# Kernel optimization log

Hardware: AMD Instinct MI355X
Metric: run time of the kernel (lower is better)

The kernel has to match this reference:

```python
import jax, jax.numpy as jnp
import numpy as np

INF = 1.0e7   # matches torch INF = 1.0 * 10000000.0
EOS_ID = 2
FIN_INIT = -1.0e9  # finite stand-in for torch's -inf init of fin_log_probs


def setup_inputs() -> dict:
    key = jax.random.key(0)
    k1, k2, k3, k4, k5, k6 = jax.random.split(key, 6)
    P, D, S, V = 32, 8, 2048, 128000
    # next-token probability distribution per (prompt, draft)
    logits = jax.random.normal(k1, (P * D, V), dtype=jnp.float32)
    probs = jax.nn.softmax(logits, axis=-1)
    alive_seq = jax.random.randint(k2, (P, D, S), 0, V, dtype=jnp.int32)
    fin_seq = jax.random.randint(k3, (P, D, S), 0, V, dtype=jnp.int32)
    alive_log_probs = -5.0 * jax.random.uniform(k4, (P, D), dtype=jnp.float32)
    fin_log_probs = jnp.full((P, D), FIN_INIT, dtype=jnp.float32)
    still_prompt = jax.random.randint(k5, (P,), 0, 2) == 1
    is_first = jax.random.randint(k6, (P,), 0, 2) == 1
    return {"probs": probs, "alive_seq": alive_seq, "fin_seq": fin_seq,
            "alive_log_probs": alive_log_probs, "fin_log_probs": fin_log_probs,
            "still_prompt": still_prompt, "is_first": is_first, "cur_pos": 1024}


def reference(probs, alive_seq, fin_seq, alive_log_probs, fin_log_probs,
              still_prompt, is_first, cur_pos):
    P, D = alive_log_probs.shape
    V = probs.shape[-1]
    # log-prob accumulation (smoothing=None path)
    log_probs = jnp.log(probs.reshape(P, D, V))                  # (P, D, V)
    curr = alive_log_probs[:, :, None] + log_probs               # (P, D, V)
    # joint topk over beams*vocab
    flat = curr.reshape(P, D * V)
    topk_lp, topk_i = jax.lax.top_k(flat, 2 * D)                 # (P, 2D)
    topk_beam_id = topk_i // V
    topk_tok = topk_i % V
    # first-generation override: only beam 0 counts
    f_vals, f_idx = jax.lax.top_k(log_probs[:, 0, :], 2 * D)     # (P, 2D)
    m = is_first[:, None]
    topk_tok = jnp.where(m, f_idx, topk_tok)
    topk_lp = jnp.where(m, alive_log_probs[:, 0:1] + f_vals, topk_lp)
    # gather parent sequences, write new token at cur_pos
    topk_seq = jnp.take_along_axis(alive_seq, topk_beam_id[:, :, None], axis=1)
    topk_seq = topk_seq.at[:, :, cur_pos].set(topk_tok)
    topk_finished = topk_tok == EOS_ID
    # grow_alive: keep best unfinished
    alive_masked = topk_lp + topk_finished * (-INF)
    na_lp, na_idx = jax.lax.top_k(alive_masked, D)               # (P, D)
    na_seq = jnp.take_along_axis(topk_seq, na_idx[:, :, None], axis=1)
    attention_change_ids = jnp.take_along_axis(topk_beam_id, na_idx, axis=1)
    # grow_fin: keep best finished among old + new
    fin_masked = topk_lp + (~topk_finished) * (-INF)
    cat_seq = jnp.concatenate([fin_seq, topk_seq], axis=1)       # (P, 3D, S)
    cat_lp = jnp.concatenate([fin_log_probs, fin_masked], axis=1)
    nf_lp, nf_idx = jax.lax.top_k(cat_lp, D)
    nf_seq = jnp.take_along_axis(cat_seq, nf_idx[:, :, None], axis=1)
    # still-prompt masking: keep old state, identity attention ids
    sp = still_prompt
    attention_change_ids = jnp.where(sp[:, None], jnp.arange(D), attention_change_ids)
    new_alive_seq = jnp.where(sp[:, None, None], alive_seq, na_seq)
    new_alive_lp = jnp.where(sp[:, None], alive_log_probs, na_lp)
    new_fin_seq = jnp.where(sp[:, None, None], fin_seq, nf_seq)
    new_fin_lp = jnp.where(sp[:, None], fin_log_probs, nf_lp)
    return (attention_change_ids, new_alive_seq, new_alive_lp, new_fin_seq, new_fin_lp)
```

## Files before the change

### kernel.cpp

```cpp
#include <hip/hip_runtime.h>
#include <stdint.h>

#define NEG_BIG -3.0e38f
#define INF_ 10000000.0f
#define EOS_ID 2
#define V_DIM 128000
#define S_DIM 2048
#define CAP 2048

__device__ __forceinline__ bool better(float v1, int i1, float v2, int i2) {
    return (v1 > v2) || (v1 == v2 && i1 < i2);
}
__device__ __forceinline__ float bf16_up(uint16_t u) {
    return __uint_as_float(((uint32_t)u) << 16);
}

__global__ __launch_bounds__(1024) void rowtopk_kernel(const void* probs,
    const uint32_t* finlp, float* ws_val, int* ws_idx) {
    const int r = blockIdx.x;
    const int t = threadIdx.x;
    const int wave = t >> 6, lane = t & 63;
    const bool isbf16 = (finlp[0] == 0xCE6ECE6Eu);

    __shared__ int s_etop, s_B, s_ncand;
    __shared__ uint32_t s_part[16][4];
    __shared__ uint32_t s_bins[8];
    __shared__ uint32_t s_cv[CAP];
    __shared__ int s_ci[CAP];

    const uint4* rowb = (const uint4*)((const uint16_t*)probs + (size_t)r * V_DIM);
    const float4* rowf = (const float4*)((const float*)probs + (size_t)r * V_DIM);
    const int nvec_b = V_DIM / 8;
    const int nvec_f = V_DIM / 4;

    if (t < 64) {
        uint32_t m = 0;
        if (isbf16) {
            uint4 q = rowb[t];
            uint32_t wd[4] = {q.x, q.y, q.z, q.w};
            #pragma unroll
            for (int c = 0; c < 4; ++c) {
                uint32_t lo = wd[c] << 16;
                uint32_t hi = wd[c] & 0xFFFF0000u;
                m = lo > m ? lo : m;
                m = hi > m ? hi : m;
            }
        } else {
            float4 q = rowf[t];
            uint32_t a = __float_as_uint(q.x), b = __float_as_uint(q.y);
            uint32_t c = __float_as_uint(q.z), d = __float_as_uint(q.w);
            m = a > m ? a : m; m = b > m ? b : m;
            m = c > m ? c : m; m = d > m ? d : m;
        }
        #pragma unroll
        for (int s = 1; s < 64; s <<= 1) {
            uint32_t o = (uint32_t)__shfl_xor((int)m, s, 64);
            m = o > m ? o : m;
        }
        if (t == 0) {
            int ea = (int)((m >> 23) & 0xFF);
            s_etop = ea + 3 > 254 ? 254 : ea + 3;
        }
    }
    __syncthreads();

    for (int attempt = 0; attempt < 6; ++attempt) {
        if (t < 64) ((uint32_t*)s_part)[t] = 0;
        if (t == 0) s_B = -1;
        __syncthreads();
        const int etop = s_etop;
        unsigned long long c0 = 0;
        if (isbf16) {
            for (int pos = t; pos < nvec_b; pos += 1024) {
                uint4 q = rowb[pos];
                uint32_t wd[4] = {q.x, q.y, q.z, q.w};
                #pragma unroll
                for (int c = 0; c < 4; ++c) {
                    int e0 = (int)((wd[c] >> 7) & 0xFF);
                    int e1 = (int)(wd[c] >> 23);
                    int k0 = etop - e0; k0 = k0 < 0 ? 0 : (k0 > 7 ? 7 : k0);
                    int k1 = etop - e1; k1 = k1 < 0 ? 0 : (k1 > 7 ? 7 : k1);
                    c0 += 1ull << (k0 << 3);
                    c0 += 1ull << (k1 << 3);
                }
            }
        } else {
            for (int pos = t; pos < nvec_f; pos += 1024) {
                float4 q = rowf[pos];
                uint32_t u[4] = {__float_as_uint(q.x), __float_as_uint(q.y),
                                 __float_as_uint(q.z), __float_as_uint(q.w)};
                #pragma unroll
                for (int c = 0; c < 4; ++c) {
                    int e = (int)(u[c] >> 23);
                    int k = etop - e; k = k < 0 ? 0 : (k > 7 ? 7 : k);
                    c0 += 1ull << (k << 3);
                }
            }
        }
        uint32_t f0 = (uint32_t)(c0 & 0xFF)         | (((uint32_t)(c0 >> 8)  & 0xFF) << 16);
        uint32_t f1 = ((uint32_t)(c0 >> 16) & 0xFF) | (((uint32_t)(c0 >> 24) & 0xFF) << 16);
        uint32_t f2 = ((uint32_t)(c0 >> 32) & 0xFF) | (((uint32_t)(c0 >> 40) & 0xFF) << 16);
        uint32_t f3 = ((uint32_t)(c0 >> 48) & 0xFF) | (((uint32_t)(c0 >> 56) & 0xFF) << 16);
        #pragma unroll
        for (int s = 1; s < 64; s <<= 1) {
            f0 += (uint32_t)__shfl_xor((int)f0, s, 64);
            f1 += (uint32_t)__shfl_xor((int)f1, s, 64);
            f2 += (uint32_t)__shfl_xor((int)f2, s, 64);
            f3 += (uint32_t)__shfl_xor((int)f3, s, 64);
        }
        if (lane == 0) {
            s_part[wave][0] = f0; s_part[wave][1] = f1;
            s_part[wave][2] = f2; s_part[wave][3] = f3;
        }
        __syncthreads();
        if (t < 8) {
            uint32_t s = 0;
            for (int w = 0; w < 16; ++w)
                s += (s_part[w][t >> 1] >> ((t & 1) * 16)) & 0xFFFFu;
            s_bins[t] = s;
        }
        __syncthreads();
        if (t == 0) {
            uint32_t cum = 0; int B = -1;
            for (int b = 0; b < 7; ++b) {
                cum += s_bins[b];
                if (cum >= 16) { B = b; break; }
            }
            if (B >= 0) s_B = B; else s_etop = etop - 7;
        }
        __syncthreads();
        if (s_B >= 0) break;
    }

    if (t == 0) s_ncand = 0;
    __syncthreads();
    int ethr = s_etop - s_B; if (ethr < 0) ethr = 0;
    const uint32_t thr = (uint32_t)ethr << 23;
    if (isbf16) {
        for (int pos = t; pos < nvec_b; pos += 1024) {
            uint4 q = rowb[pos];
            uint32_t wd[4] = {q.x, q.y, q.z, q.w};
            #pragma unroll
            for (int c = 0; c < 4; ++c) {
                uint32_t lo = wd[c] << 16;
                uint32_t hi = wd[c] & 0xFFFF0000u;
                if (lo >= thr) {
                    int slot = atomicAdd(&s_ncand, 1);
                    if (slot < CAP) { s_cv[slot] = lo; s_ci[slot] = pos * 8 + c * 2; }
                }
                if (hi >= thr) {
                    int slot = atomicAdd(&s_ncand, 1);
                    if (slot < CAP) { s_cv[slot] = hi; s_ci[slot] = pos * 8 + c * 2 + 1; }
                }
            }
        }
    } else {
        for (int pos = t; pos < nvec_f; pos += 1024) {
            float4 q = rowf[pos];
            uint32_t u[4] = {__float_as_uint(q.x), __float_as_uint(q.y),
                             __float_as_uint(q.z), __float_as_uint(q.w)};
            #pragma unroll
            for (int c = 0; c < 4; ++c) {
                if (u[c] >= thr) {
                    int slot = atomicAdd(&s_ncand, 1);
                    if (slot < CAP) { s_cv[slot] = u[c]; s_ci[slot] = pos * 4 + c; }
                }
            }
        }
    }
    __syncthreads();
    const int C = s_ncand < CAP ? s_ncand : CAP;

    if (t < 64) {
        uint32_t taken = 0;
        for (int k = 0; k < 16; ++k) {
            float bv = NEG_BIG; int bi = 0x7fffffff; int bs = -1;
            int q = 0;
            for (int j = lane; j < C; j += 64, ++q) {
                if ((taken >> q) & 1u) continue;
                float v = __uint_as_float(s_cv[j]);
                int ix = s_ci[j];
                if (better(v, ix, bv, bi)) { bv = v; bi = ix; bs = j; }
            }
            #pragma unroll
            for (int m = 1; m < 64; m <<= 1) {
                float ov = __shfl_xor(bv, m, 64);
                int oi = __shfl_xor(bi, m, 64);
                int os = __shfl_xor(bs, m, 64);
                if (better(ov, oi, bv, bi)) { bv = ov; bi = oi; bs = os; }
            }
            if (bs >= 0 && (bs & 63) == lane) taken |= 1u << (bs >> 6);
            if (lane == 0) { ws_val[r * 16 + k] = bv; ws_idx[r * 16 + k] = bi; }
        }
    }
}

__global__ __launch_bounds__(64) void select_kernel(
    const void* alive_lp_p, const void* fin_lp_p,
    const uint32_t* spw, const uint32_t* isfw,
    const float* ws_val, const int* ws_idx,
    int2* desc, float* out) {
    const int p = blockIdx.x;
    const int t = threadIdx.x;
    const int lane = t;

    __shared__ float cv[128]; __shared__ int cflat[128];
    __shared__ float s_alive_lp[8]; __shared__ float s_fin_lp[8];
    __shared__ float topk_lp[16]; __shared__ int topk_tok[16]; __shared__ int topk_beam[16];
    __shared__ int na_sel[8]; __shared__ float na_val[8];
    __shared__ int nf_sel[8]; __shared__ float nf_val[8];

    const bool isbf16 = (((const uint32_t*)fin_lp_p)[0] == 0xCE6ECE6Eu);
    uint32_t w1 = (t < 8) ? spw[t] : 0u;
    uint32_t w2 = (t < 8) ? isfw[t] : 0u;
    const bool bbyte = (__ballot(w1 > 1u || w2 > 1u) != 0ull);

    const bool sp  = bbyte ? (((const uint8_t*)spw)[p] != 0) : (spw[p] != 0u);
    const bool isf = bbyte ? (((const uint8_t*)isfw)[p] != 0) : (isfw[p] != 0u);

    if (t < 8) {
        float a, f;
        if (isbf16) {
            a = bf16_up(((const uint16_t*)alive_lp_p)[p * 8 + t]);
            f = bf16_up(((const uint16_t*)fin_lp_p)[p * 8 + t]);
        } else {
            a = ((const float*)alive_lp_p)[p * 8 + t];
            f = ((const float*)fin_lp_p)[p * 8 + t];
        }
        s_alive_lp[t] = a; s_fin_lp[t] = f;
    }
    __syncthreads();

    for (int i = t; i < 128; i += 64) {
        int d = i >> 4, m = i & 15;
        int r = p * 8 + d;
        cv[i] = s_alive_lp[d] + logf(ws_val[r * 16 + m]);
        cflat[i] = d * V_DIM + ws_idx[r * 16 + m];
    }
    __syncthreads();

    {
        bool taken0 = false, taken1 = false;
        for (int k = 0; k < 16; ++k) {
            float v0 = taken0 ? NEG_BIG : cv[lane];
            int   f0 = taken0 ? 0x7fffffff : cflat[lane];
            float v1 = taken1 ? NEG_BIG : cv[lane + 64];
            int   f1 = taken1 ? 0x7fffffff : cflat[lane + 64];
            float bv; int bf, bj;
            if (better(v0, f0, v1, f1)) { bv = v0; bf = f0; bj = lane; }
            else                        { bv = v1; bf = f1; bj = lane + 64; }
            #pragma unroll
            for (int m = 1; m < 64; m <<= 1) {
                float ov = __shfl_xor(bv, m, 64);
                int   of = __shfl_xor(bf, m, 64);
                int   oj = __shfl_xor(bj, m, 64);
                if (better(ov, of, bv, bf)) { bv = ov; bf = of; bj = oj; }
            }
            if (bj == lane)      taken0 = true;
            if (bj == lane + 64) taken1 = true;
            if (lane == 0) {
                topk_lp[k]   = bv;
                topk_beam[k] = bf / V_DIM;
                topk_tok[k]  = bf % V_DIM;
            }
        }
    }
    __syncthreads();

    if (isf && t < 16) {
        int r0 = p * 8;
        topk_tok[t] = ws_idx[r0 * 16 + t];
        topk_lp[t]  = s_alive_lp[0] + logf(ws_val[r0 * 16 + t]);
    }
    __syncthreads();

    {
        float mv = NEG_BIG; int mi = 0x7fffffff;
        if (lane < 16) {
            mv = topk_lp[lane] + ((topk_tok[lane] == EOS_ID) ? -INF_ : 0.0f);
            mi = lane;
        }
        bool taken = false;
        for (int k = 0; k < 8; ++k) {
            float bv = taken ? NEG_BIG : mv;
            int   bi = taken ? 0x7fffffff : mi;
            #pragma unroll
            for (int m = 1; m < 64; m <<= 1) {
                float ov = __shfl_xor(bv, m, 64);
                int   oi = __shfl_xor(bi, m, 64);
                if (better(ov, oi, bv, bi)) { bv = ov; bi = oi; }
            }
            if (lane < 16 && bi == mi) taken = true;
            if (lane == 0) { na_sel[k] = bi; na_val[k] = bv; }
        }
    }
    {
        float fv = NEG_BIG; int fi = 0x7fffffff;
        if (lane < 8) { fv = s_fin_lp[lane]; fi = lane; }
        else if (lane < 24) {
            int j = lane - 8;
            fv = topk_lp[j] + ((topk_tok[j] == EOS_ID) ? 0.0f : -INF_);
            fi = lane;
        }
        bool taken = false;
        for (int k = 0; k < 8; ++k) {
            float bv = taken ? NEG_BIG : fv;
            int   bi = taken ? 0x7fffffff : fi;
            #pragma unroll
            for (int m = 1; m < 64; m <<= 1) {
                float ov = __shfl_xor(bv, m, 64);
                int   oi = __shfl_xor(bi, m, 64);
                if (better(ov, oi, bv, bi)) { bv = ov; bi = oi; }
            }
            if (lane < 24 && bi == fi) taken = true;
            if (lane == 0) { nf_sel[k] = bi; nf_val[k] = bv; }
        }
    }
    __syncthreads();

    float* out_attn = out;
    float* out_alp  = out + 256 + 524288;
    float* out_flp  = out + 512 + 2 * 524288;
    if (t < 8) {
        int k = t;
        int na = na_sel[k], nf = nf_sel[k];
        out_attn[p * 8 + k] = (float)(sp ? k : topk_beam[na]);
        out_alp[p * 8 + k]  = sp ? s_alive_lp[k] : na_val[k];
        out_flp[p * 8 + k]  = sp ? s_fin_lp[k]   : nf_val[k];

        int a_src, a_patch, f_src, f_patch;
        if (sp) {
            a_src = p * 8 + k;               a_patch = -1;
            f_src = (p * 8 + k) | (1 << 30); f_patch = -1;
        } else {
            a_src = p * 8 + topk_beam[na];   a_patch = topk_tok[na];
            if (nf < 8) { f_src = (p * 8 + nf) | (1 << 30); f_patch = -1; }
            else { int j = nf - 8; f_src = p * 8 + topk_beam[j]; f_patch = topk_tok[j]; }
        }
        desc[p * 8 + k]       = make_int2(a_src, a_patch);
        desc[256 + p * 8 + k] = make_int2(f_src, f_patch);
    }
}

__global__ __launch_bounds__(256) void copy_kernel(const int* alive_seq, const int* fin_seq,
                                                   const int* cur_pos_p, const int2* desc,
                                                   float* out) {
    const int bi = blockIdx.x;
    const int arr = bi >> 8;
    const int rk = bi & 255;
    int2 d = desc[arr * 256 + rk];
    const int src = d.x, patch = d.y;
    const int* s = ((src >> 30) & 1) ? fin_seq : alive_seq;
    const int4* srow = (const int4*)(s + (size_t)(src & 0x3FFFFFFF) * S_DIM);
    float* drow = out + (arr ? (512 + 524288) : 256) + (size_t)rk * S_DIM;
    const int cp = cur_pos_p[0];

    for (int i = threadIdx.x; i < S_DIM / 4; i += 256) {
        int4 v = srow[i];
        if (patch >= 0) {
            int s0 = i * 4;
            if (s0 + 0 == cp) v.x = patch;
            if (s0 + 1 == cp) v.y = patch;
            if (s0 + 2 == cp) v.z = patch;
            if (s0 + 3 == cp) v.w = patch;
        }
        float4 f = make_float4((float)v.x, (float)v.y, (float)v.z, (float)v.w);
        ((float4*)drow)[i] = f;
    }
}

extern "C" void kernel_launch(void* const* d_in, const int* in_sizes, int n_in,
                              void* d_out, int out_size, void* d_ws, size_t ws_size,
                              hipStream_t stream) {
    (void)in_sizes; (void)n_in; (void)out_size; (void)ws_size;
    const void* probs      = d_in[0];
    const int*  alive_seq  = (const int*)d_in[1];
    const int*  fin_seq    = (const int*)d_in[2];
    const void* alive_lp   = d_in[3];
    const void* fin_lp     = d_in[4];
    const uint32_t* spw    = (const uint32_t*)d_in[5];
    const uint32_t* isfw   = (const uint32_t*)d_in[6];
    const int*  cur_pos    = (const int*)d_in[7];

    float* ws_val = (float*)d_ws;
    int*   ws_idx = (int*)((char*)d_ws + 16384);
    int2*  desc   = (int2*)((char*)d_ws + 32768);

    rowtopk_kernel<<<256, 1024, 0, stream>>>(probs, (const uint32_t*)fin_lp, ws_val, ws_idx);
    select_kernel<<<32, 64, 0, stream>>>(alive_lp, fin_lp, spw, isfw,
                                         ws_val, ws_idx, desc, (float*)d_out);
    copy_kernel<<<512, 256, 0, stream>>>(alive_seq, fin_seq, cur_pos, desc, (float*)d_out);
}
```

Baseline: 253.3 us.

## Fuse select into copy kernel and unroll row-scan loads for more memory parallelism

The histogram and filter passes of the row top-k kernel are manually unrolled so each thread issues four independent 16-byte loads before processing them, raising memory-level parallelism on the 128k-wide rows. The separate select and copy kernels are merged into one 512-block kernel in which every block redundantly recomputes its prompt's beam selection and then copies its own sequence row. This removes one launch and the descriptor round-trip through workspace, at the cost of repeating the small selection work in every block. The unrolled histogram loops hardcode trip counts that assume V=128000.

```diff
diff --git a/kernel.cpp b/kernel.cpp
--- a/kernel.cpp
+++ b/kernel.cpp
@@ -13,6 +13,29 @@
 }
 __device__ __forceinline__ float bf16_up(uint16_t u) {
     return __uint_as_float(((uint32_t)u) << 16);
+}
+
+__device__ __forceinline__ void hist_b16(uint4 q, int etop, unsigned long long& c0) {
+    uint32_t wd[4] = {q.x, q.y, q.z, q.w};
+    #pragma unroll
+    for (int c = 0; c < 4; ++c) {
+        int e0 = (int)((wd[c] >> 7) & 0xFF);
+        int e1 = (int)(wd[c] >> 23);
+        int k0 = etop - e0; k0 = k0 < 0 ? 0 : (k0 > 7 ? 7 : k0);
+        int k1 = etop - e1; k1 = k1 < 0 ? 0 : (k1 > 7 ? 7 : k1);
+        c0 += 1ull << (k0 << 3);
+        c0 += 1ull << (k1 << 3);
+    }
+}
+__device__ __forceinline__ void hist_f32(float4 q, int etop, unsigned long long& c0) {
+    uint32_t u[4] = {__float_as_uint(q.x), __float_as_uint(q.y),
+                     __float_as_uint(q.z), __float_as_uint(q.w)};
+    #pragma unroll
+    for (int c = 0; c < 4; ++c) {
+        int e = (int)(u[c] >> 23);
+        int k = etop - e; k = k < 0 ? 0 : (k > 7 ? 7 : k);
+        c0 += 1ull << (k << 3);
+    }
 }
 
 __global__ __launch_bounds__(1024) void rowtopk_kernel(const void* probs,
@@ -71,30 +94,24 @@
         const int etop = s_etop;
         unsigned long long c0 = 0;
         if (isbf16) {
-            for (int pos = t; pos < nvec_b; pos += 1024) {
-                uint4 q = rowb[pos];
-                uint32_t wd[4] = {q.x, q.y, q.z, q.w};
-                #pragma unroll
-                for (int c = 0; c < 4; ++c) {
-                    int e0 = (int)((wd[c] >> 7) & 0xFF);
-                    int e1 = (int)(wd[c] >> 23);
-                    int k0 = etop - e0; k0 = k0 < 0 ? 0 : (k0 > 7 ? 7 : k0);
-                    int k1 = etop - e1; k1 = k1 < 0 ? 0 : (k1 > 7 ? 7 : k1);
-                    c0 += 1ull << (k0 << 3);
-                    c0 += 1ull << (k1 << 3);
-                }
+            #pragma unroll
+            for (int j = 0; j < 2; ++j) {
+                uint4 q0 = rowb[t + 8192 * j];
+                uint4 q1 = rowb[t + 8192 * j + 2048];
+                uint4 q2 = rowb[t + 8192 * j + 4096];
+                uint4 q3 = rowb[t + 8192 * j + 6144];
+                hist_b16(q0, etop, c0); hist_b16(q1, etop, c0);
+                hist_b16(q2, etop, c0); hist_b16(q3, etop, c0);
             }
         } else {
-            for (int pos = t; pos < nvec_f; pos += 1024) {
-                float4 q = rowf[pos];
-                uint32_t u[4] = {__float_as_uint(q.x), __float_as_uint(q.y),
-                                 __float_as_uint(q.z), __float_as_uint(q.w)};
-                #pragma unroll
-                for (int c = 0; c < 4; ++c) {
-                    int e = (int)(u[c] >> 23);
-                    int k = etop - e; k = k < 0 ? 0 : (k > 7 ? 7 : k);
-                    c0 += 1ull << (k << 3);
-                }
+            #pragma unroll
+            for (int j = 0; j < 4; ++j) {
+                float4 q0 = rowf[t + 8192 * j];
+                float4 q1 = rowf[t + 8192 * j + 2048];
+                float4 q2 = rowf[t + 8192 * j + 4096];
+                float4 q3 = rowf[t + 8192 * j + 6144];
+                hist_f32(q0, etop, c0); hist_f32(q1, etop, c0);
+                hist_f32(q2, etop, c0); hist_f32(q3, etop, c0);
             }
         }
         uint32_t f0 = (uint32_t)(c0 & 0xFF)         | (((uint32_t)(c0 >> 8)  & 0xFF) << 16);
@@ -136,36 +153,59 @@
     __syncthreads();
     int ethr = s_etop - s_B; if (ethr < 0) ethr = 0;
     const uint32_t thr = (uint32_t)ethr << 23;
+
     if (isbf16) {
-        for (int pos = t; pos < nvec_b; pos += 1024) {
+        #define FILT_B(qv, basepos)                                             \
+        {   uint32_t wd[4] = {(qv).x, (qv).y, (qv).z, (qv).w};                  \
+            _Pragma("unroll")                                                   \
+            for (int c = 0; c < 4; ++c) {                                       \
+                uint32_t lo = wd[c] << 16;                                      \
+                uint32_t hi = wd[c] & 0xFFFF0000u;                              \
+                if (lo >= thr) {                                                \
+                    int slot = atomicAdd(&s_ncand, 1);                          \
+                    if (slot < CAP) { s_cv[slot] = lo; s_ci[slot] = (basepos) * 8 + c * 2; } \
+                }                                                               \
+                if (hi >= thr) {                                                \
+                    int slot = atomicAdd(&s_ncand, 1);                          \
+                    if (slot < CAP) { s_cv[slot] = hi; s_ci[slot] = (basepos) * 8 + c * 2 + 1; } \
+                }                                                               \
+            }                                                                   \
+        }
+        for (int base = 0; base < 12288; base += 4096) {
+            uint4 q0 = rowb[base + t];
+            uint4 q1 = rowb[base + t + 1024];
+            uint4 q2 = rowb[base + t + 2048];
+            uint4 q3 = rowb[base + t + 3072];
+            FILT_B(q0, base + t); FILT_B(q1, base + t + 1024);
+            FILT_B(q2, base + t + 2048); FILT_B(q3, base + t + 3072);
+        }
+        for (int pos = 12288 + t; pos < nvec_b; pos += 1024) {
             uint4 q = rowb[pos];
-            uint32_t wd[4] = {q.x, q.y, q.z, q.w};
-            #pragma unroll
-            for (int c = 0; c < 4; ++c) {
-                uint32_t lo = wd[c] << 16;
-                uint32_t hi = wd[c] & 0xFFFF0000u;
-                if (lo >= thr) {
-                    int slot = atomicAdd(&s_ncand, 1);
-                    if (slot < CAP) { s_cv[slot] = lo; s_ci[slot] = pos * 8 + c * 2; }
-                }
-                if (hi >= thr) {
-                    int slot = atomicAdd(&s_ncand, 1);
-                    if (slot < CAP) { s_cv[slot] = hi; s_ci[slot] = pos * 8 + c * 2 + 1; }
-                }
-            }
+            FILT_B(q, pos);
         }
     } else {
-        for (int pos = t; pos < nvec_f; pos += 1024) {
+        #define FILT_F(qv, basepos)                                             \
+        {   uint32_t u[4] = {__float_as_uint((qv).x), __float_as_uint((qv).y),  \
+                             __float_as_uint((qv).z), __float_as_uint((qv).w)}; \
+            _Pragma("unroll")                                                   \
+            for (int c = 0; c < 4; ++c) {                                       \
+                if (u[c] >= thr) {                                              \
+                    int slot = atomicAdd(&s_ncand, 1);                          \
+                    if (slot < CAP) { s_cv[slot] = u[c]; s_ci[slot] = (basepos) * 4 + c; } \
+                }                                                               \
+            }                                                                   \
+        }
+        for (int base = 0; base < 28672; base += 4096) {
+            float4 q0 = rowf[base + t];
+            float4 q1 = rowf[base + t + 1024];
+            float4 q2 = rowf[base + t + 2048];
+            float4 q3 = rowf[base + t + 3072];
+            FILT_F(q0, base + t); FILT_F(q1, base + t + 1024);
+            FILT_F(q2, base + t + 2048); FILT_F(q3, base + t + 3072);
+        }
+        for (int pos = 28672 + t; pos < nvec_f; pos += 1024) {
             float4 q = rowf[pos];
-            uint32_t u[4] = {__float_as_uint(q.x), __float_as_uint(q.y),
-                             __float_as_uint(q.z), __float_as_uint(q.w)};
-            #pragma unroll
-            for (int c = 0; c < 4; ++c) {
-                if (u[c] >= thr) {
-                    int slot = atomicAdd(&s_ncand, 1);
-                    if (slot < CAP) { s_cv[slot] = u[c]; s_ci[slot] = pos * 4 + c; }
-                }
-            }
+            FILT_F(q, pos);
         }
     }
     __syncthreads();
@@ -195,24 +235,28 @@
     }
 }
 
-__global__ __launch_bounds__(64) void select_kernel(
+__global__ __launch_bounds__(256) void selcopy_kernel(
     const void* alive_lp_p, const void* fin_lp_p,
-    const uint32_t* spw, const uint32_t* isfw,
-    const float* ws_val, const int* ws_idx,
-    int2* desc, float* out) {
-    const int p = blockIdx.x;
+    const int* alive_seq, const int* fin_seq,
+    const uint32_t* spw, const uint32_t* isfw, const int* cur_pos_p,
+    const float* ws_val, const int* ws_idx, float* out) {
+    const int bi = blockIdx.x;
+    const int arr = bi >> 8;
+    const int rk = bi & 255;
+    const int p = rk >> 3, kk = rk & 7;
     const int t = threadIdx.x;
-    const int lane = t;
+    const int lane = t & 63;
 
     __shared__ float cv[128]; __shared__ int cflat[128];
     __shared__ float s_alive_lp[8]; __shared__ float s_fin_lp[8];
     __shared__ float topk_lp[16]; __shared__ int topk_tok[16]; __shared__ int topk_beam[16];
     __shared__ int na_sel[8]; __shared__ float na_val[8];
     __shared__ int nf_sel[8]; __shared__ float nf_val[8];
+    __shared__ int s_src, s_patch;
 
     const bool isbf16 = (((const uint32_t*)fin_lp_p)[0] == 0xCE6ECE6Eu);
-    uint32_t w1 = (t < 8) ? spw[t] : 0u;
-    uint32_t w2 = (t < 8) ? isfw[t] : 0u;
+    uint32_t w1 = (lane < 8) ? spw[lane] : 0u;
+    uint32_t w2 = (lane < 8) ? isfw[lane] : 0u;
     const bool bbyte = (__ballot(w1 > 1u || w2 > 1u) != 0ull);
 
     const bool sp  = bbyte ? (((const uint8_t*)spw)[p] != 0) : (spw[p] != 0u);
@@ -231,15 +275,15 @@
     }
     __syncthreads();
 
-    for (int i = t; i < 128; i += 64) {
-        int d = i >> 4, m = i & 15;
+    if (t < 128) {
+        int d = t >> 4, m = t & 15;
         int r = p * 8 + d;
-        cv[i] = s_alive_lp[d] + logf(ws_val[r * 16 + m]);
-        cflat[i] = d * V_DIM + ws_idx[r * 16 + m];
-    }
-    __syncthreads();
-
-    {
+        cv[t] = s_alive_lp[d] + logf(ws_val[r * 16 + m]);
+        cflat[t] = d * V_DIM + ws_idx[r * 16 + m];
+    }
+    __syncthreads();
+
+    if (t < 64) {
         bool taken0 = false, taken1 = false;
         for (int k = 0; k < 16; ++k) {
             float v0 = taken0 ? NEG_BIG : cv[lane];
@@ -274,46 +318,48 @@
     }
     __syncthreads();
 
-    {
-        float mv = NEG_BIG; int mi = 0x7fffffff;
-        if (lane < 16) {
-            mv = topk_lp[lane] + ((topk_tok[lane] == EOS_ID) ? -INF_ : 0.0f);
-            mi = lane;
-        }
-        bool taken = false;
-        for (int k = 0; k < 8; ++k) {
-            float bv = taken ? NEG_BIG : mv;
-            int   bi = taken ? 0x7fffffff : mi;
-            #pragma unroll
-            for (int m = 1; m < 64; m <<= 1) {
-                float ov = __shfl_xor(bv, m, 64);
-                int   oi = __shfl_xor(bi, m, 64);
-                if (better(ov, oi, bv, bi)) { bv = ov; bi = oi; }
-            }
-            if (lane < 16 && bi == mi) taken = true;
-            if (lane == 0) { na_sel[k] = bi; na_val[k] = bv; }
-        }
-    }
-    {
-        float fv = NEG_BIG; int fi = 0x7fffffff;
-        if (lane < 8) { fv = s_fin_lp[lane]; fi = lane; }
-        else if (lane < 24) {
-            int j = lane - 8;
-            fv = topk_lp[j] + ((topk_tok[j] == EOS_ID) ? 0.0f : -INF_);
-            fi = lane;
-        }
-        bool taken = false;
-        for (int k = 0; k < 8; ++k) {
-            float bv = taken ? NEG_BIG : fv;
-            int   bi = taken ? 0x7fffffff : fi;
-            #pragma unroll
-            for (int m = 1; m < 64; m <<= 1) {
-                float ov = __shfl_xor(bv, m, 64);
-                int   oi = __shfl_xor(bi, m, 64);
-                if (better(ov, oi, bv, bi)) { bv = ov; bi = oi; }
-            }
-            if (lane < 24 && bi == fi) taken = true;
-            if (lane == 0) { nf_sel[k] = bi; nf_val[k] = bv; }
+    if (t < 64) {
+        {
+            float mv = NEG_BIG; int mi = 0x7fffffff;
+            if (lane < 16) {
+                mv = topk_lp[lane] + ((topk_tok[lane] == EOS_ID) ? -INF_ : 0.0f);
+                mi = lane;
+            }
+            bool taken = false;
+            for (int k = 0; k < 8; ++k) {
+                float bv = taken ? NEG_BIG : mv;
+                int   bix = taken ? 0x7fffffff : mi;
+                #pragma unroll
+                for (int m = 1; m < 64; m <<= 1) {
+                    float ov = __shfl_xor(bv, m, 64);
+                    int   oi = __shfl_xor(bix, m, 64);
+                    if (better(ov, oi, bv, bix)) { bv = ov; bix = oi; }
+                }
+                if (lane < 16 && bix == mi) taken = true;
+                if (lane == 0) { na_sel[k] = bix; na_val[k] = bv; }
+            }
+        }
+        {
+            float fv = NEG_BIG; int fi = 0x7fffffff;
+            if (lane < 8) { fv = s_fin_lp[lane]; fi = lane; }
+            else if (lane < 24) {
+                int j = lane - 8;
+                fv = topk_lp[j] + ((topk_tok[j] == EOS_ID) ? 0.0f : -INF_);
+                fi = lane;
+            }
+            bool taken = false;
+            for (int k = 0; k < 8; ++k) {
+                float bv = taken ? NEG_BIG : fv;
+                int   bix = taken ? 0x7fffffff : fi;
+                #pragma unroll
+                for (int m = 1; m < 64; m <<= 1) {
+                    float ov = __shfl_xor(bv, m, 64);
+                    int   oi = __shfl_xor(bix, m, 64);
+                    if (better(ov, oi, bv, bix)) { bv = ov; bix = oi; }
+                }
+                if (lane < 24 && bix == fi) taken = true;
+                if (lane == 0) { nf_sel[k] = bix; nf_val[k] = bv; }
+            }
         }
     }
     __syncthreads();
@@ -321,41 +367,33 @@
     float* out_attn = out;
     float* out_alp  = out + 256 + 524288;
     float* out_flp  = out + 512 + 2 * 524288;
-    if (t < 8) {
-        int k = t;
-        int na = na_sel[k], nf = nf_sel[k];
-        out_attn[p * 8 + k] = (float)(sp ? k : topk_beam[na]);
-        out_alp[p * 8 + k]  = sp ? s_alive_lp[k] : na_val[k];
-        out_flp[p * 8 + k]  = sp ? s_fin_lp[k]   : nf_val[k];
-
-        int a_src, a_patch, f_src, f_patch;
-        if (sp) {
-            a_src = p * 8 + k;               a_patch = -1;
-            f_src = (p * 8 + k) | (1 << 30); f_patch = -1;
+    if (t == 0) {
+        int na = na_sel[kk], nf = nf_sel[kk];
+        if (arr == 0) {
+            out_attn[p * 8 + kk] = (float)(sp ? kk : topk_beam[na]);
+            out_alp[p * 8 + kk]  = sp ? s_alive_lp[kk] : na_val[kk];
+            out_flp[p * 8 + kk]  = sp ? s_fin_lp[kk]   : nf_val[kk];
+        }
+        int src, patch;
+        if (arr == 0) {
+            if (sp) { src = p * 8 + kk; patch = -1; }
+            else    { src = p * 8 + topk_beam[na]; patch = topk_tok[na]; }
         } else {
-            a_src = p * 8 + topk_beam[na];   a_patch = topk_tok[na];
-            if (nf < 8) { f_src = (p * 8 + nf) | (1 << 30); f_patch = -1; }
-            else { int j = nf - 8; f_src = p * 8 + topk_beam[j]; f_patch = topk_tok[j]; }
-        }
-        desc[p * 8 + k]       = make_int2(a_src, a_patch);
-        desc[256 + p * 8 + k] = make_int2(f_src, f_patch);
-    }
-}
-
-__global__ __launch_bounds__(256) void copy_kernel(const int* alive_seq, const int* fin_seq,
-                                                   const int* cur_pos_p, const int2* desc,
-                                                   float* out) {
-    const int bi = blockIdx.x;
-    const int arr = bi >> 8;
-    const int rk = bi & 255;
-    int2 d = desc[arr * 256 + rk];
-    const int src = d.x, patch = d.y;
+            if (sp) { src = (p * 8 + kk) | (1 << 30); patch = -1; }
+            else if (nf < 8) { src = (p * 8 + nf) | (1 << 30); patch = -1; }
+            else { int j = nf - 8; src = p * 8 + topk_beam[j]; patch = topk_tok[j]; }
+        }
+        s_src = src; s_patch = patch;
+    }
+    __syncthreads();
+
+    const int src = s_src, patch = s_patch;
     const int* s = ((src >> 30) & 1) ? fin_seq : alive_seq;
     const int4* srow = (const int4*)(s + (size_t)(src & 0x3FFFFFFF) * S_DIM);
     float* drow = out + (arr ? (512 + 524288) : 256) + (size_t)rk * S_DIM;
     const int cp = cur_pos_p[0];
 
-    for (int i = threadIdx.x; i < S_DIM / 4; i += 256) {
+    for (int i = t; i < S_DIM / 4; i += 256) {
         int4 v = srow[i];
         if (patch >= 0) {
             int s0 = i * 4;
@@ -364,8 +402,7 @@
             if (s0 + 2 == cp) v.z = patch;
             if (s0 + 3 == cp) v.w = patch;
         }
-        float4 f = make_float4((float)v.x, (float)v.y, (float)v.z, (float)v.w);
-        ((float4*)drow)[i] = f;
+        ((float4*)drow)[i] = make_float4((float)v.x, (float)v.y, (float)v.z, (float)v.w);
     }
 }
 
@@ -384,10 +421,9 @@
 
     float* ws_val = (float*)d_ws;
     int*   ws_idx = (int*)((char*)d_ws + 16384);
-    int2*  desc   = (int2*)((char*)d_ws + 32768);
 
     rowtopk_kernel<<<256, 1024, 0, stream>>>(probs, (const uint32_t*)fin_lp, ws_val, ws_idx);
-    select_kernel<<<32, 64, 0, stream>>>(alive_lp, fin_lp, spw, isfw,
-                                         ws_val, ws_idx, desc, (float*)d_out);
-    copy_kernel<<<512, 256, 0, stream>>>(alive_seq, fin_seq, cur_pos, desc, (float*)d_out);
-}
+    selcopy_kernel<<<512, 256, 0, stream>>>(alive_lp, fin_lp, alive_seq, fin_seq,
+                                            spw, isfw, cur_pos, ws_val, ws_idx,
+                                            (float*)d_out);
+}
```

After: 235.2 us. 7.1% less time.
